# Kernel tuning notes

Hardware: AMD Instinct MI355X
Metric: run time of the kernel (lower is better)

Reference implementation:

```python
import jax, jax.numpy as jnp
import numpy as np

N_NODES = 20000
N_EDGES = 320000
F_IN, HID, OUT = 128, 256, 32
N_LAYERS = 30
N_GRAPHS = 16


def setup_inputs() -> dict:
    key = jax.random.key(0)
    ks = jax.random.split(key, 10)
    x = jax.random.normal(ks[0], (N_NODES, F_IN), dtype=jnp.float32)
    edge_list = jax.random.randint(ks[1], (2, N_EDGES), 0, N_NODES, dtype=jnp.int64)
    batch = jnp.sort(jax.random.randint(ks[2], (N_NODES,), 0, N_GRAPHS, dtype=jnp.int64))
    # GCNConv weights: conv1, 29 middle layers, final linear
    W1 = jax.random.normal(ks[3], (F_IN, HID), dtype=jnp.float32) / np.sqrt(F_IN)
    b1 = jnp.zeros((HID,), dtype=jnp.float32)
    Wm = jax.random.normal(ks[4], (N_LAYERS - 1, HID, HID), dtype=jnp.float32) / np.sqrt(HID)
    bm = jnp.zeros((N_LAYERS - 1, HID), dtype=jnp.float32)
    Wlin = jax.random.normal(ks[5], (HID, OUT), dtype=jnp.float32) / np.sqrt(HID)
    blin = jnp.zeros((OUT,), dtype=jnp.float32)
    return {"x": x, "edge_list": edge_list, "batch": batch,
            "W1": W1, "b1": b1, "Wm": Wm, "bm": bm, "Wlin": Wlin, "blin": blin}


def reference(x, edge_list, batch, W1, b1, Wm, bm, Wlin, blin):
    n = x.shape[0]
    loop = jnp.arange(n, dtype=edge_list.dtype)
    src = jnp.concatenate([edge_list[0], loop])  # senders (+ self loops)
    dst = jnp.concatenate([edge_list[1], loop])  # receivers (+ self loops)
    # symmetric GCN normalization: deg counted at receivers incl. self loops
    deg = jax.ops.segment_sum(jnp.ones_like(dst, dtype=x.dtype), dst, num_segments=n)
    dinv = jnp.where(deg > 0, jax.lax.rsqrt(deg), 0.0)
    norm = dinv[src] * dinv[dst]  # [E+n]

    def conv(h, W, b):
        h = h @ W  # dense linear first (PyG GCNConv)
        agg = jax.ops.segment_sum(h[src] * norm[:, None], dst, num_segments=n)
        return jax.nn.relu(agg + b)

    h = conv(x, W1, b1)

    def step(h, wb):
        W, b = wb
        return conv(h, W, b), None

    h, _ = jax.lax.scan(step, h, (Wm, bm))

    # global mean pool over graphs
    counts = jax.ops.segment_sum(jnp.ones((n,), x.dtype), batch, num_segments=N_GRAPHS)
    pooled = jax.ops.segment_sum(h, batch, num_segments=N_GRAPHS) / jnp.maximum(counts, 1.0)[:, None]
    return pooled @ Wlin + blin
```

## Files before the change

kernel.cpp:

```cpp
#include <hip/hip_runtime.h>

typedef unsigned short u16;
typedef unsigned int u32;
typedef __attribute__((ext_vector_type(8))) _Float16 f16x8;
typedef __attribute__((ext_vector_type(4))) float f32x4;
typedef __attribute__((ext_vector_type(8))) u16 u16x8;

#define N_NODES 20000
#define N_EDGES 320000
#define F_IN 128
#define HID 256
#define OUT_F 32
#define N_LAYERS 30
#define N_GRAPHS 16
#define ELLCAP 64

__device__ __forceinline__ float h2f(u16 u) {
    _Float16 h;
    __builtin_memcpy(&h, &u, 2);
    return (float)h;
}
__device__ __forceinline__ u16 f2h(float f) {
    _Float16 h = (_Float16)f;
    u16 u;
    __builtin_memcpy(&u, &h, 2);
    return u;
}

__device__ __forceinline__ void gl_lds16(const u16* g, u16* l) {
    __builtin_amdgcn_global_load_lds((const u32*)g, (u32*)l, 16, 0, 0);
}

__global__ void fill_ell_kernel(const int* __restrict__ src, const int* __restrict__ dst,
                                int* __restrict__ cursor, u16* __restrict__ ell_col, int E) {
    int e = blockIdx.x * blockDim.x + threadIdx.x;
    if (e >= E) return;
    int s = src[e], d = dst[e];
    int slot = atomicAdd(&cursor[d], 1);
    if (slot < ELLCAP) ell_col[d * ELLCAP + slot] = (u16)s;
}

__global__ void dinv_kernel(const int* __restrict__ cnt, float* __restrict__ dinv, int n) {
    int i = blockIdx.x * blockDim.x + threadIdx.x;
    if (i < n) dinv[i] = rsqrtf((float)(cnt[i] + 1));
}

__global__ void prescale_x_kernel(const float* __restrict__ x, const int* __restrict__ cnt,
                                  u16* __restrict__ xs, int total) {
    int i = blockIdx.x * 256 + threadIdx.x;
    if (i < total) xs[i] = f2h(x[i] * rsqrtf((float)(cnt[i >> 7] + 1)));
}

__global__ __launch_bounds__(256) void transpose_f16_tiled(const float* __restrict__ W,
                                                           u16* __restrict__ T,
                                                           int K, int N) {
    __shared__ float tile[32][33];
    const int l = blockIdx.y;
    const int ntn = N >> 5;
    const int kt = blockIdx.x / ntn, ntile = blockIdx.x % ntn;
    const float* Wl = W + (size_t)l * K * N;
    u16* Tl = T + (size_t)l * K * N;
    const int r8 = threadIdx.x >> 5, c = threadIdx.x & 31;
    #pragma unroll
    for (int rr = 0; rr < 4; ++rr) {
        int r = rr * 8 + r8;
        tile[r][c] = Wl[(size_t)(kt * 32 + r) * N + ntile * 32 + c];
    }
    __syncthreads();
    #pragma unroll
    for (int rr = 0; rr < 4; ++rr) {
        int n = rr * 8 + r8;
        float v = tile[c][n];
        Tl[(size_t)(ntile * 32 + n) * K + kt * 32 + c] = f2h(v);
    }
}

template <int K>
__global__ __launch_bounds__(256, 3) void layer_fused(const u16* __restrict__ hs,
                                                      const u16* __restrict__ B,
                                                      const u16* __restrict__ ell_col,
                                                      const int* __restrict__ cnt,
                                                      const float* __restrict__ dinv,
                                                      const float* __restrict__ bias,
                                                      const float* __restrict__ rowscale,
                                                      u16* __restrict__ Ch,
                                                      float* __restrict__ C) {
    __shared__ u16 cols[32 * ELLCAP];
    __shared__ __align__(16) u16 gs[32 * K];
    __shared__ __align__(16) u16 Bs[256 * 64];
    const int node0 = blockIdx.x * 32;
    const int tid = threadIdx.x;
    *(u16x8*)&cols[tid * 8] = *(const u16x8*)&ell_col[(size_t)node0 * ELLCAP + tid * 8];
    const int nd = tid >> 3, sub = tid & 7;
    const int node = node0 + nd;
    int c = cnt[node]; c = c < ELLCAP ? c : ELLCAP;
    const float dd = dinv[node];
    __syncthreads();
    const u16* cl = &cols[nd * ELLCAP];
    const int nb = (c + 7) >> 3;

    #pragma unroll 1
    for (int p = 0; p < K / 64; ++p) {
        const int f = p * 64 + sub * 8;
        f32x4 a0 = {}, a1 = {};
        {
            u16x8 sv = *(const u16x8*)(hs + (size_t)node * K + f);
            #pragma unroll
            for (int i = 0; i < 4; ++i) a0[i] += h2f(sv[i]);
            #pragma unroll
            for (int i = 0; i < 4; ++i) a1[i] += h2f(sv[i + 4]);
        }
        if (nb > 0) {
            u16x8 vbuf[8];
            u16x8 cc = *(const u16x8*)&cl[0];
            #pragma unroll
            for (int j = 0; j < 8; ++j) vbuf[j] = *(const u16x8*)(hs + (size_t)cc[j] * K + f);
            int base = 0;
            for (int b = 1; b < nb; ++b) {
                u16x8 cn = *(const u16x8*)&cl[b * 8];
                u16x8 vn[8];
                #pragma unroll
                for (int j = 0; j < 8; ++j) vn[j] = *(const u16x8*)(hs + (size_t)cn[j] * K + f);
                #pragma unroll
                for (int j = 0; j < 8; ++j) {
                    #pragma unroll
                    for (int i = 0; i < 4; ++i) a0[i] += h2f(vbuf[j][i]);
                    #pragma unroll
                    for (int i = 0; i < 4; ++i) a1[i] += h2f(vbuf[j][i + 4]);
                }
                base += 8;
                #pragma unroll
                for (int j = 0; j < 8; ++j) vbuf[j] = vn[j];
            }
            const u16x8 zz = {};
            #pragma unroll
            for (int j = 0; j < 8; ++j) {
                u16x8 v = (base + j < c) ? vbuf[j] : zz;
                #pragma unroll
                for (int i = 0; i < 4; ++i) a0[i] += h2f(v[i]);
                #pragma unroll
                for (int i = 0; i < 4; ++i) a1[i] += h2f(v[i + 4]);
            }
        }
        u16x8 o;
        #pragma unroll
        for (int i = 0; i < 4; ++i) o[i] = f2h(a0[i] * dd);
        #pragma unroll
        for (int i = 0; i < 4; ++i) o[i + 4] = f2h(a1[i] * dd);
        const int cc_ = p * 8 + sub;
        *(u16x8*)&gs[nd * K + ((cc_ ^ (nd & 7)) << 3)] = o;
    }

    const int wave = tid >> 6, lane = tid & 63;
    const int lr = lane >> 3, lc = lane & 7;
    #pragma unroll
    for (int q = 0; q < 8; ++q) {
        int rl = (wave * 8 + q) * 8 + lr;
        gl_lds16(B + (size_t)rl * K + ((lc ^ (rl & 7)) << 3), &Bs[(wave * 8 + q) * 512]);
    }
    f32x4 acc[2][4] = {};
    #pragma unroll
    for (int k = 0; k < K / 64; ++k) {
        __syncthreads();
        const int k0 = k * 64;
        #pragma unroll
        for (int kk = 0; kk < 2; ++kk) {
            const int c8 = kk * 4 + (lane >> 4);
            f16x8 bf[4];
            #pragma unroll
            for (int nt = 0; nt < 4; ++nt) {
                int n = wave * 64 + nt * 16 + (lane & 15);
                bf[nt] = *(const f16x8*)&Bs[n * 64 + ((c8 ^ (n & 7)) << 3)];
            }
            #pragma unroll
            for (int mt = 0; mt < 2; ++mt) {
                int ml = mt * 16 + (lane & 15);
                int cg = (k0 >> 3) + c8;
                f16x8 af = *(const f16x8*)&gs[ml * K + ((cg ^ (ml & 7)) << 3)];
                #pragma unroll
                for (int nt = 0; nt < 4; ++nt)
                    acc[mt][nt] = __builtin_amdgcn_mfma_f32_16x16x32_f16(af, bf[nt], acc[mt][nt], 0, 0, 0);
            }
        }
        if (k + 1 < K / 64) {
            __syncthreads();
            const int kn = k0 + 64;
            #pragma unroll
            for (int q = 0; q < 8; ++q) {
                int rl = (wave * 8 + q) * 8 + lr;
                gl_lds16(B + (size_t)rl * K + kn + ((lc ^ (rl & 7)) << 3), &Bs[(wave * 8 + q) * 512]);
            }
        }
    }
    #pragma unroll
    for (int mt = 0; mt < 2; ++mt) {
        int gr = node0 + mt * 16 + ((lane >> 4) << 2);
        #pragma unroll
        for (int r = 0; r < 4; ++r) {
            float sc = rowscale ? rowscale[gr + r] : 1.f;
            #pragma unroll
            for (int nt = 0; nt < 4; ++nt) {
                int gc = wave * 64 + nt * 16 + (lane & 15);
                float v = sc * fmaxf(acc[mt][nt][r] + bias[gc], 0.f);
                if (Ch) Ch[(size_t)(gr + r) * HID + gc] = f2h(v);
                else    C[(size_t)(gr + r) * HID + gc] = v;
            }
        }
    }
}

#define POOL_CHUNK 32
__global__ __launch_bounds__(256) void pool_kernel(const float* __restrict__ h,
                                                   const int* __restrict__ batch,
                                                   float* __restrict__ pool_sum) {
    int f = threadIdx.x;
    int start = blockIdx.x * POOL_CHUNK;
    int end = start + POOL_CHUNK; end = end < N_NODES ? end : N_NODES;
    if (start >= N_NODES) return;
    int gcur = batch[start];
    float acc = 0.f;
    for (int i = start; i < end; ++i) {
        int g = batch[i];
        if (g != gcur) { atomicAdd(&pool_sum[gcur * HID + f], acc); acc = 0.f; gcur = g; }
        acc += h[(size_t)i * HID + f];
    }
    atomicAdd(&pool_sum[gcur * HID + f], acc);
}

__device__ int lb_int(const int* __restrict__ a, int n, int v) {
    int lo = 0, hi = n;
    while (lo < hi) {
        int mid = (lo + hi) >> 1;
        if (a[mid] < v) lo = mid + 1; else hi = mid;
    }
    return lo;
}

__global__ void final_linear_kernel(const float* __restrict__ pool_sum,
                                    const int* __restrict__ batch,
                                    const float* __restrict__ Wlin,
                                    const float* __restrict__ blin,
                                    float* __restrict__ out) {
    int idx = blockIdx.x * blockDim.x + threadIdx.x;
    if (idx >= N_GRAPHS * OUT_F) return;
    int g = idx / OUT_F, o = idx % OUT_F;
    int lo = lb_int(batch, N_NODES, g);
    int hi = lb_int(batch, N_NODES, g + 1);
    float cinv = 1.f / fmaxf((float)(hi - lo), 1.f);
    float s = blin[o];
    for (int k = 0; k < HID; ++k) s += (pool_sum[g * HID + k] * cinv) * Wlin[k * OUT_F + o];
    out[idx] = s;
}

static inline size_t align_up(size_t x, size_t a) { return (x + a - 1) & ~(a - 1); }

extern "C" void kernel_launch(void* const* d_in, const int* in_sizes, int n_in,
                              void* d_out, int out_size, void* d_ws, size_t ws_size,
                              hipStream_t stream) {
    const float* x     = (const float*)d_in[0];
    const int*   elist = (const int*)d_in[1];
    const int*   batch = (const int*)d_in[2];
    const float* W1    = (const float*)d_in[3];
    const float* b1    = (const float*)d_in[4];
    const float* Wm    = (const float*)d_in[5];
    const float* bm    = (const float*)d_in[6];
    const float* Wlin  = (const float*)d_in[7];
    const float* blin  = (const float*)d_in[8];
    float* outp = (float*)d_out;

    const int* srcA = elist;
    const int* dstA = elist + N_EDGES;

    char* ws = (char*)d_ws;
    size_t off = 0;
    float* h      = (float*)(ws + off); off = align_up(off + sizeof(float) * N_NODES * HID, 1024);
    u16*   hA     = (u16*)(ws + off);   off = align_up(off + sizeof(u16) * N_NODES * HID, 1024);
    u16*   hB     = (u16*)(ws + off);   off = align_up(off + sizeof(u16) * N_NODES * HID, 1024);
    u16*   xs     = (u16*)(ws + off);   off = align_up(off + sizeof(u16) * N_NODES * F_IN, 1024);
    u16*   W1T    = (u16*)(ws + off);   off = align_up(off + sizeof(u16) * F_IN * HID, 1024);
    u16*   WmT    = (u16*)(ws + off);   off = align_up(off + sizeof(u16) * (N_LAYERS - 1) * HID * HID, 1024);
    int*   cursor = (int*)(ws + off);   off = align_up(off + sizeof(int) * N_NODES, 1024);
    float* dinv   = (float*)(ws + off); off = align_up(off + sizeof(float) * N_NODES, 1024);
    u16*   ell_col = (u16*)(ws + off);  off = align_up(off + sizeof(u16) * N_NODES * ELLCAP, 1024);
    float* pool_sum = (float*)(ws + off); off = align_up(off + sizeof(float) * N_GRAPHS * HID, 1024);

    hipMemsetAsync(cursor, 0, sizeof(int) * N_NODES, stream);
    hipMemsetAsync(ell_col, 0, sizeof(u16) * N_NODES * ELLCAP, stream);
    hipMemsetAsync(pool_sum, 0, sizeof(float) * N_GRAPHS * HID, stream);

    fill_ell_kernel<<<(N_EDGES + 255) / 256, 256, 0, stream>>>(srcA, dstA, cursor, ell_col, N_EDGES);
    dinv_kernel<<<(N_NODES + 255) / 256, 256, 0, stream>>>(cursor, dinv, N_NODES);
    prescale_x_kernel<<<(N_NODES * F_IN + 255) / 256, 256, 0, stream>>>(x, cursor, xs, N_NODES * F_IN);

    transpose_f16_tiled<<<dim3((F_IN / 32) * (HID / 32), 1), 256, 0, stream>>>(W1, W1T, F_IN, HID);
    transpose_f16_tiled<<<dim3((HID / 32) * (HID / 32), N_LAYERS - 1), 256, 0, stream>>>(Wm, WmT, HID, HID);

    const int lgrid = N_NODES / 32;
    layer_fused<F_IN><<<lgrid, 256, 0, stream>>>(xs, W1T, ell_col, cursor, dinv, b1, dinv, hA, h);
    u16* cur = hA; u16* nxt = hB;
    for (int l = 0; l < N_LAYERS - 1; ++l) {
        const bool last = (l == N_LAYERS - 2);
        layer_fused<HID><<<lgrid, 256, 0, stream>>>(cur, WmT + (size_t)l * HID * HID,
                                                    ell_col, cursor, dinv,
                                                    bm + (size_t)l * HID,
                                                    last ? nullptr : dinv,
                                                    last ? nullptr : nxt, h);
        u16* t = cur; cur = nxt; nxt = t;
    }
    pool_kernel<<<(N_NODES + POOL_CHUNK - 1) / POOL_CHUNK, 256, 0, stream>>>(h, batch, pool_sum);
    final_linear_kernel<<<2, 256, 0, stream>>>(pool_sum, batch, Wlin, blin, outp);
}
```

Baseline: 930.9 us.

## Interleave gather and MFMA per 64-wide K chunk to shrink LDS and raise occupancy

Restructures the fused layer kernel so each 64-feature chunk is gathered, written to a small LDS tile, and immediately multiplied against the matching B slice, instead of gathering all K features first and then running the GEMM. This cuts the gs LDS buffer from 32*K to 32*64 elements and raises the launch bound to 4 blocks per CU. The double-buffered neighbor gather loop is also simplified to a single-buffered one, which reduces register use but gives up software prefetch of neighbor rows. Extra barriers per chunk and the loss of load/compute overlap may offset the occupancy gain.

```diff
diff --git a/kernel.cpp b/kernel.cpp
--- a/kernel.cpp
+++ b/kernel.cpp
@@ -76,7 +76,7 @@
 }
 
 template <int K>
-__global__ __launch_bounds__(256, 3) void layer_fused(const u16* __restrict__ hs,
+__global__ __launch_bounds__(256, 4) void layer_fused(const u16* __restrict__ hs,
                                                       const u16* __restrict__ B,
                                                       const u16* __restrict__ ell_col,
                                                       const int* __restrict__ cnt,
@@ -86,7 +86,7 @@
                                                       u16* __restrict__ Ch,
                                                       float* __restrict__ C) {
     __shared__ u16 cols[32 * ELLCAP];
-    __shared__ __align__(16) u16 gs[32 * K];
+    __shared__ __align__(16) u16 gs[32 * 64];
     __shared__ __align__(16) u16 Bs[256 * 64];
     const int node0 = blockIdx.x * 32;
     const int tid = threadIdx.x;
@@ -95,13 +95,22 @@
     const int node = node0 + nd;
     int c = cnt[node]; c = c < ELLCAP ? c : ELLCAP;
     const float dd = dinv[node];
+    const int wave = tid >> 6, lane = tid & 63;
+    const int lr = lane >> 3, lc = lane & 7;
+    f32x4 acc[2][4] = {};
     __syncthreads();
     const u16* cl = &cols[nd * ELLCAP];
     const int nb = (c + 7) >> 3;
 
     #pragma unroll 1
     for (int p = 0; p < K / 64; ++p) {
-        const int f = p * 64 + sub * 8;
+        const int kb = p * 64;
+        #pragma unroll
+        for (int q = 0; q < 8; ++q) {
+            int rl = (wave * 8 + q) * 8 + lr;
+            gl_lds16(B + (size_t)rl * K + kb + ((lc ^ (rl & 7)) << 3), &Bs[(wave * 8 + q) * 512]);
+        }
+        const int f = kb + sub * 8;
         f32x4 a0 = {}, a1 = {};
         {
             u16x8 sv = *(const u16x8*)(hs + (size_t)node * K + f);
@@ -110,36 +119,33 @@
             #pragma unroll
             for (int i = 0; i < 4; ++i) a1[i] += h2f(sv[i + 4]);
         }
+        for (int b = 0; b < nb - 1; ++b) {
+            u16x8 cc = *(const u16x8*)&cl[b * 8];
+            u16x8 v[8];
+            #pragma unroll
+            for (int j = 0; j < 8; ++j) v[j] = *(const u16x8*)(hs + (size_t)cc[j] * K + f);
+            #pragma unroll
+            for (int j = 0; j < 8; ++j) {
+                #pragma unroll
+                for (int i = 0; i < 4; ++i) a0[i] += h2f(v[j][i]);
+                #pragma unroll
+                for (int i = 0; i < 4; ++i) a1[i] += h2f(v[j][i + 4]);
+            }
+        }
         if (nb > 0) {
-            u16x8 vbuf[8];
-            u16x8 cc = *(const u16x8*)&cl[0];
-            #pragma unroll
-            for (int j = 0; j < 8; ++j) vbuf[j] = *(const u16x8*)(hs + (size_t)cc[j] * K + f);
-            int base = 0;
-            for (int b = 1; b < nb; ++b) {
-                u16x8 cn = *(const u16x8*)&cl[b * 8];
-                u16x8 vn[8];
-                #pragma unroll
-                for (int j = 0; j < 8; ++j) vn[j] = *(const u16x8*)(hs + (size_t)cn[j] * K + f);
-                #pragma unroll
-                for (int j = 0; j < 8; ++j) {
-                    #pragma unroll
-                    for (int i = 0; i < 4; ++i) a0[i] += h2f(vbuf[j][i]);
-                    #pragma unroll
-                    for (int i = 0; i < 4; ++i) a1[i] += h2f(vbuf[j][i + 4]);
-                }
-                base += 8;
-                #pragma unroll
-                for (int j = 0; j < 8; ++j) vbuf[j] = vn[j];
-            }
+            const int base = (nb - 1) * 8;
+            u16x8 cc = *(const u16x8*)&cl[base];
+            u16x8 v[8];
+            #pragma unroll
+            for (int j = 0; j < 8; ++j) v[j] = *(const u16x8*)(hs + (size_t)cc[j] * K + f);
             const u16x8 zz = {};
             #pragma unroll
             for (int j = 0; j < 8; ++j) {
-                u16x8 v = (base + j < c) ? vbuf[j] : zz;
-                #pragma unroll
-                for (int i = 0; i < 4; ++i) a0[i] += h2f(v[i]);
-                #pragma unroll
-                for (int i = 0; i < 4; ++i) a1[i] += h2f(v[i + 4]);
+                u16x8 vv = (base + j < c) ? v[j] : zz;
+                #pragma unroll
+                for (int i = 0; i < 4; ++i) a0[i] += h2f(vv[i]);
+                #pragma unroll
+                for (int i = 0; i < 4; ++i) a1[i] += h2f(vv[i + 4]);
             }
         }
         u16x8 o;
@@ -147,22 +153,9 @@
         for (int i = 0; i < 4; ++i) o[i] = f2h(a0[i] * dd);
         #pragma unroll
         for (int i = 0; i < 4; ++i) o[i + 4] = f2h(a1[i] * dd);
-        const int cc_ = p * 8 + sub;
-        *(u16x8*)&gs[nd * K + ((cc_ ^ (nd & 7)) << 3)] = o;
-    }
-
-    const int wave = tid >> 6, lane = tid & 63;
-    const int lr = lane >> 3, lc = lane & 7;
-    #pragma unroll
-    for (int q = 0; q < 8; ++q) {
-        int rl = (wave * 8 + q) * 8 + lr;
-        gl_lds16(B + (size_t)rl * K + ((lc ^ (rl & 7)) << 3), &Bs[(wave * 8 + q) * 512]);
-    }
-    f32x4 acc[2][4] = {};
-    #pragma unroll
-    for (int k = 0; k < K / 64; ++k) {
+        *(u16x8*)&gs[nd * 64 + ((sub ^ (nd & 7)) << 3)] = o;
+
         __syncthreads();
-        const int k0 = k * 64;
         #pragma unroll
         for (int kk = 0; kk < 2; ++kk) {
             const int c8 = kk * 4 + (lane >> 4);
@@ -175,22 +168,13 @@
             #pragma unroll
             for (int mt = 0; mt < 2; ++mt) {
                 int ml = mt * 16 + (lane & 15);
-                int cg = (k0 >> 3) + c8;
-                f16x8 af = *(const f16x8*)&gs[ml * K + ((cg ^ (ml & 7)) << 3)];
+                f16x8 af = *(const f16x8*)&gs[ml * 64 + ((c8 ^ (ml & 7)) << 3)];
                 #pragma unroll
                 for (int nt = 0; nt < 4; ++nt)
                     acc[mt][nt] = __builtin_amdgcn_mfma_f32_16x16x32_f16(af, bf[nt], acc[mt][nt], 0, 0, 0);
             }
         }
-        if (k + 1 < K / 64) {
-            __syncthreads();
-            const int kn = k0 + 64;
-            #pragma unroll
-            for (int q = 0; q < 8; ++q) {
-                int rl = (wave * 8 + q) * 8 + lr;
-                gl_lds16(B + (size_t)rl * K + kn + ((lc ^ (rl & 7)) << 3), &Bs[(wave * 8 + q) * 512]);
-            }
-        }
+        __syncthreads();
     }
     #pragma unroll
     for (int mt = 0; mt < 2; ++mt) {
```

New measurement: 1.301 ms. +39.8%, slower.

## Double-buffer weight tiles in LDS and prefetch first tile before aggregation

Applied to the files above, without the earlier changes.

Splits the weight staging buffer into two 32-wide K slices that are double-buffered. The next slice is loaded asynchronously while MFMAs run on the current one, which removes one barrier per step. The first weight slice is now issued before the neighbor aggregation phase, so its latency overlaps the gather. LDS footprint stays the same, but there are twice as many K iterations and the swizzle changes to 4-way, which may add bank conflicts.

```diff
diff --git a/kernel.cpp b/kernel.cpp
--- a/kernel.cpp
+++ b/kernel.cpp
@@ -87,7 +87,7 @@
                                                       float* __restrict__ C) {
     __shared__ u16 cols[32 * ELLCAP];
     __shared__ __align__(16) u16 gs[32 * K];
-    __shared__ __align__(16) u16 Bs[256 * 64];
+    __shared__ __align__(16) u16 Bs[2][256 * 32];
     const int node0 = blockIdx.x * 32;
     const int tid = threadIdx.x;
     *(u16x8*)&cols[tid * 8] = *(const u16x8*)&ell_col[(size_t)node0 * ELLCAP + tid * 8];
@@ -95,9 +95,18 @@
     const int node = node0 + nd;
     int c = cnt[node]; c = c < ELLCAP ? c : ELLCAP;
     const float dd = dinv[node];
+    const int wave = tid >> 6, lane = tid & 63;
+    const int r4 = lane >> 2, ch = lane & 3;
+    constexpr int S = K / 32;
     __syncthreads();
     const u16* cl = &cols[nd * ELLCAP];
     const int nb = (c + 7) >> 3;
+
+    #pragma unroll
+    for (int q = 0; q < 4; ++q) {
+        int rl = wave * 64 + q * 16 + r4;
+        gl_lds16(B + (size_t)rl * K + ((ch ^ (r4 & 3)) << 3), &Bs[0][(wave * 4 + q) * 512]);
+    }
 
     #pragma unroll 1
     for (int p = 0; p < K / 64; ++p) {
@@ -151,45 +160,34 @@
         *(u16x8*)&gs[nd * K + ((cc_ ^ (nd & 7)) << 3)] = o;
     }
 
-    const int wave = tid >> 6, lane = tid & 63;
-    const int lr = lane >> 3, lc = lane & 7;
-    #pragma unroll
-    for (int q = 0; q < 8; ++q) {
-        int rl = (wave * 8 + q) * 8 + lr;
-        gl_lds16(B + (size_t)rl * K + ((lc ^ (rl & 7)) << 3), &Bs[(wave * 8 + q) * 512]);
-    }
     f32x4 acc[2][4] = {};
     #pragma unroll
-    for (int k = 0; k < K / 64; ++k) {
+    for (int k = 0; k < S; ++k) {
         __syncthreads();
-        const int k0 = k * 64;
-        #pragma unroll
-        for (int kk = 0; kk < 2; ++kk) {
-            const int c8 = kk * 4 + (lane >> 4);
-            f16x8 bf[4];
-            #pragma unroll
-            for (int nt = 0; nt < 4; ++nt) {
-                int n = wave * 64 + nt * 16 + (lane & 15);
-                bf[nt] = *(const f16x8*)&Bs[n * 64 + ((c8 ^ (n & 7)) << 3)];
+        if (k + 1 < S) {
+            #pragma unroll
+            for (int q = 0; q < 4; ++q) {
+                int rl = wave * 64 + q * 16 + r4;
+                gl_lds16(B + (size_t)rl * K + (k + 1) * 32 + ((ch ^ (r4 & 3)) << 3),
+                         &Bs[(k + 1) & 1][(wave * 4 + q) * 512]);
             }
-            #pragma unroll
-            for (int mt = 0; mt < 2; ++mt) {
-                int ml = mt * 16 + (lane & 15);
-                int cg = (k0 >> 3) + c8;
-                f16x8 af = *(const f16x8*)&gs[ml * K + ((cg ^ (ml & 7)) << 3)];
-                #pragma unroll
-                for (int nt = 0; nt < 4; ++nt)
-                    acc[mt][nt] = __builtin_amdgcn_mfma_f32_16x16x32_f16(af, bf[nt], acc[mt][nt], 0, 0, 0);
-            }
-        }
-        if (k + 1 < K / 64) {
-            __syncthreads();
-            const int kn = k0 + 64;
-            #pragma unroll
-            for (int q = 0; q < 8; ++q) {
-                int rl = (wave * 8 + q) * 8 + lr;
-                gl_lds16(B + (size_t)rl * K + kn + ((lc ^ (rl & 7)) << 3), &Bs[(wave * 8 + q) * 512]);
-            }
+        }
+        const u16* Bk = Bs[k & 1];
+        const int c8 = lane >> 4;
+        f16x8 bf[4];
+        #pragma unroll
+        for (int nt = 0; nt < 4; ++nt) {
+            int n = wave * 64 + nt * 16 + (lane & 15);
+            bf[nt] = *(const f16x8*)&Bk[(wave * 4 + nt) * 512 + (((n & 15) * 4 + (c8 ^ (n & 3))) << 3)];
+        }
+        #pragma unroll
+        for (int mt = 0; mt < 2; ++mt) {
+            int ml = mt * 16 + (lane & 15);
+            int cg = k * 4 + c8;
+            f16x8 af = *(const f16x8*)&gs[ml * K + ((cg ^ (ml & 7)) << 3)];
+            #pragma unroll
+            for (int nt = 0; nt < 4; ++nt)
+                acc[mt][nt] = __builtin_amdgcn_mfma_f32_16x16x32_f16(af, bf[nt], acc[mt][nt], 0, 0, 0);
         }
     }
     #pragma unroll
```

Measured after the change: 952.5 us. +2.3%, slower.
